# Performance work log

Measured on AMD Instinct MI355X. Metric: run time of the kernel, lower is better.

The kernel has to match this reference:

```python
import jax, jax.numpy as jnp
import numpy as np
from jax import lax

T, B, E = 512, 128, 128  # timesteps, batch, embedding_size
S = 2 * T                # stack capacity: 2 pushes per step


def setup_inputs() -> dict:
    key = jax.random.key(0)
    k1, k2, k3, k4, k5 = jax.random.split(key, 5)
    return {
        "v1": jax.random.normal(k1, (T, B, E), dtype=jnp.float32),
        "v2": jax.random.normal(k2, (T, B, E), dtype=jnp.float32),
        "d1": jax.random.uniform(k3, (T, B, 1), dtype=jnp.float32),
        "d2": jax.random.uniform(k4, (T, B, 1), dtype=jnp.float32),
        "u": jax.random.uniform(k5, (T, B, 1), dtype=jnp.float32),
    }


def _step(carry, xs):
    strengths, values = carry  # [B,S], [B,S,E]; slots 0..2(t+1)-1 valid after push
    v1t, v2t, d1t, d2t, ut, t = xs  # v*: [B,E]; d*,u: [B,1]; t: scalar int
    # --- push: append two entries at the top (slots 2t, 2t+1) ---
    values = lax.dynamic_update_slice(
        values, jnp.stack([v1t, v2t], axis=1), (0, 2 * t, 0))
    strengths = lax.dynamic_update_slice(
        strengths, jnp.concatenate([d1t, d2t], axis=1), (0, 2 * t))
    # exclusive reverse cumsum = strength used above each slot (top-down order)
    rev_incl = jnp.flip(jnp.cumsum(jnp.flip(strengths, 1), axis=1), 1)  # [B,S]
    used = rev_incl - strengths  # [B,S]
    # --- read: faithful to torch.max(u - strength_used) reducing over batch ---
    m = jnp.max(ut - used, axis=0)            # [S] scalar-over-batch per slot
    w = jnp.minimum(strengths, m[None, :])    # [B,S]; invalid slots hit v=0
    summary = jnp.einsum('bs,bse->be', w, values)  # [B,E]
    # --- pop: s -= min(s, relu(u - used)) using pre-pop strengths ---
    pop_amt = jnp.minimum(strengths, jnp.maximum(0.0, ut - used))
    strengths = strengths - pop_amt
    return (strengths, values), summary


def reference(v1, v2, d1, d2, u):
    init = (jnp.zeros((B, S), v1.dtype), jnp.zeros((B, S, E), v1.dtype))
    ts = jnp.arange(T, dtype=jnp.int32)
    _, out = lax.scan(_step, init, (v1, v2, d1, d2, u, ts))
    return out  # [T,B,E]: read content at each timestep
```

## Files before the change

kernel.cpp:

```cpp
#include <hip/hip_runtime.h>
#include <cstdint>
#include <cstddef>

#define TT 512
#define BB 128
#define EE 128
#define SS 1024
#define NEG_INF (-1e30f)

typedef _Float16 half8 __attribute__((ext_vector_type(8)));
typedef float floatx4 __attribute__((ext_vector_type(4)));

__device__ __forceinline__ unsigned int pkh(float x, float y) {
    _Float16 hx = (_Float16)x, hy = (_Float16)y;
    unsigned short bx, by;
    __builtin_memcpy(&bx, &hx, 2); __builtin_memcpy(&by, &hy, 2);
    return (unsigned int)bx | ((unsigned int)by << 16);
}

__device__ __forceinline__ unsigned int pkrtz(float x, float y) {
    auto h = __builtin_amdgcn_cvt_pkrtz(x, y);
    unsigned int r; __builtin_memcpy(&r, &h, 4); return r;
}

__global__ __launch_bounds__(64) void prefixF(
    const float* __restrict__ d1, const float* __restrict__ d2,
    const float* __restrict__ u,
    float* __restrict__ F, float* __restrict__ Bv,
    float* __restrict__ d2T, float* __restrict__ FT,
    float* __restrict__ BvT, float* __restrict__ CST,
    float* __restrict__ CMT, float* __restrict__ HT)
{
    const int b = blockIdx.x;
    const int lane = threadIdx.x;
    const int t0 = lane * 8;

    float l1[8], l2[8], g[8];
#pragma unroll
    for (int j = 0; j < 8; ++j) {
        const int t = t0 + j;
        l1[j] = d1[t * BB + b];
        l2[j] = d2[t * BB + b];
        g[j] = u[t * BB + b] - l1[j] - l2[j];
    }
    float p[8], s = 0.f;
#pragma unroll
    for (int j = 0; j < 8; ++j) { s += g[j]; p[j] = s; }

    float v = s;
#pragma unroll
    for (int off = 1; off < 64; off <<= 1) {
        float o = __shfl_up(v, off);
        if (lane >= off) v += o;
    }
    const float excl = v - s;

    float Fv[8];
#pragma unroll
    for (int j = 0; j < 8; ++j) Fv[j] = excl + p[j];

#pragma unroll
    for (int j = 0; j < 8; ++j) {
        const int t = t0 + j;
        const float Fm1 = (j > 0) ? Fv[j - 1] : excl;
        const float Bvv = Fm1 - l1[j];
        F  [b * TT + t] = Fv[j];
        Bv [b * TT + t] = Bvv;
        d2T[b * TT + t] = l2[j];
        FT [t * BB + b] = Fv[j];
        BvT[t * BB + b] = Bvv;
    }

    float pm[8], sm[8];
    pm[0] = Fv[0];
#pragma unroll
    for (int j = 1; j < 8; ++j) pm[j] = fmaxf(pm[j - 1], Fv[j]);
    sm[7] = Fv[7];
#pragma unroll
    for (int j = 6; j >= 0; --j) sm[j] = fmaxf(sm[j + 1], Fv[j]);

    float pcar = NEG_INF, scar = NEG_INF;
#pragma unroll
    for (int off = 1; off <= 3; ++off) {
        float xu = __shfl_up(pm[7], off);
        if ((lane & 3) >= off) pcar = fmaxf(pcar, xu);
        float xd = __shfl_down(sm[0], off);
        if ((lane & 3) + off <= 3) scar = fmaxf(scar, xd);
    }

#pragma unroll
    for (int j = 0; j < 8; ++j) {
        const int t = t0 + j;
        const float Hv  = fmaxf(pcar, (j > 0) ? pm[j - 1] : NEG_INF);
        const float CSv = fmaxf(sm[j], scar);
        HT [t * BB + b] = Hv;
        CST[t * BB + b] = CSv;
    }
    if ((lane & 3) == 0)
        CMT[(lane >> 2) * BB + b] = fmaxf(sm[0], scar);
}

__global__ __launch_bounds__(256) void calcM2(
    const float* __restrict__ FT, const float* __restrict__ BvT,
    const float* __restrict__ CST, const float* __restrict__ CMT,
    const float* __restrict__ HT, const float* __restrict__ u,
    float* __restrict__ m)
{
    const int t = (int)blockIdx.y;
    const int ci = (int)blockIdx.x;
    const int ct = t >> 5;
    if (ci > ct) return;

    const int tid = threadIdx.x;
    const int b = tid & 127, h = tid >> 7;
    const int ib = 32 * ci;

    __shared__ float cand[BB][66];
    __shared__ float Tot[2][BB];
    __shared__ float red[4][64];

    const float Ft = FT[t * BB + b];

    if (ci < ct) {
        float K = HT[t * BB + b];
        for (int c = ci + 1; c < ct; ++c) K = fmaxf(K, CMT[c * BB + b]);
#pragma unroll
        for (int j = 0; j < 16; ++j) {
            const int jj = 16 * h + j;
            const int i = ib + jj;
            const float R = fmaxf(CST[i * BB + b], K);
            const float Bvv = BvT[i * BB + b];
            cand[b][2 * jj]     = Ft - fmaxf(Bvv, R);
            cand[b][2 * jj + 1] = Ft - R;
        }
    } else {
        float vv[16], sfx[16];
#pragma unroll
        for (int j = 0; j < 16; ++j) {
            const int i = ib + 16 * h + j;
            vv[j] = (i < t) ? FT[i * BB + b] : NEG_INF;
        }
        sfx[15] = vv[15];
#pragma unroll
        for (int j = 14; j >= 0; --j) sfx[j] = fmaxf(vv[j], sfx[j + 1]);
        Tot[h][b] = sfx[0];
        __syncthreads();
        const float carry = (h == 0) ? Tot[1][b] : NEG_INF;
        const float ub = u[t * BB + b];
#pragma unroll
        for (int j = 0; j < 16; ++j) {
            const int jj = 16 * h + j;
            const int i = ib + jj;
            const float R = fmaxf(sfx[j], carry);
            const float Bvv = BvT[i * BB + b];
            cand[b][2 * jj]     = Ft - fmaxf(Bvv, R);
            cand[b][2 * jj + 1] = (i == t) ? ub : (Ft - R);
        }
    }
    __syncthreads();

    {
        const int s = tid & 63, g = tid >> 6;
        float mx = NEG_INF;
        const int b0 = g * 32;
#pragma unroll 8
        for (int bb = b0; bb < b0 + 32; ++bb) mx = fmaxf(mx, cand[bb][s]);
        red[g][s] = mx;
    }
    __syncthreads();
    if (tid < 64) {
        const float r = fmaxf(fmaxf(red[0][tid], red[1][tid]),
                              fmaxf(red[2][tid], red[3][tid]));
        const int s_glob = 64 * ci + tid;
        if (s_glob < 2 * t + 2) m[(size_t)t * SS + s_glob] = r;
    }
}

#define PWH 68
#define PWW 34
#define VTO 2176
#define FRO 6528
#define S0O 7040
#define BVO 7616
#define D2O 8128
#define TPO 8192

__global__ __launch_bounds__(256) void phaseC_mfma(
    const float* __restrict__ F, const float* __restrict__ Bvg,
    const float* __restrict__ d2T, const float* __restrict__ m,
    const float* __restrict__ v1, const float* __restrict__ v2,
    float* __restrict__ out)
{
    const int b  = blockIdx.x & (BB - 1);
    const int k8 = blockIdx.x >> 7;
    const int tt = 7 - (k8 ^ (((k8 + 2) >> 2) & 1));
    const int t0 = tt * 64;
    const int tid = threadIdx.x;

    __shared__ float sh[8256];

    const int lane = tid & 63, w = tid >> 6;
    const int wr = w >> 1, wc = w & 1;
    const int n = lane & 15;
    const int kq = (lane >> 4) * 8;
    const int il = tid & 31, g = tid >> 5;
    const int veb = tid & 7;
    const int vip = ((tid >> 3) & 7) + 8 * wc;
    const int veh = wr * 64;
    const int nchunks = 2 * tt + 2;

    float4 pv[8];
    float2 pmv[8];

    auto prefetch = [&](int ck) {
        const int ib = 32 * ck;
        const int i = ib + il;
#pragma unroll
        for (int r8 = 0; r8 < 8; ++r8) {
            const int t = t0 + 8 * g + r8;
            pmv[r8] = *(const float2*)&m[(size_t)t * SS + 2 * i];
        }
        const int i0 = ib + 2 * vip, i1 = i0 + 1;
        const float* p10 = v1 + ((size_t)i0 * BB + b) * EE;
        const float* p11 = v1 + ((size_t)i1 * BB + b) * EE;
        const float* p20 = v2 + ((size_t)i0 * BB + b) * EE;
        const float* p21 = v2 + ((size_t)i1 * BB + b) * EE;
#pragma unroll
        for (int c = 0; c < 2; ++c) {
            const int e0 = 4 * veb + 32 * c + veh;
            pv[4 * c + 0] = *(const float4*)&p10[e0];
            pv[4 * c + 1] = *(const float4*)&p11[e0];
            pv[4 * c + 2] = *(const float4*)&p20[e0];
            pv[4 * c + 3] = *(const float4*)&p21[e0];
        }
    };

    const int nF = t0 + 64;
    for (int k = tid; k < nF; k += 256) {
        sh[FRO + k] = F[b * TT + k];
        sh[BVO + k] = Bvg[b * TT + k];
    }
    if (tid < 64) sh[D2O + tid] = d2T[b * TT + t0 + tid];

    prefetch(0);

    __syncthreads();

    {
        const int k1 = tid, k2 = tid + 256, k3 = tid + 512;
        sh[S0O + k1] = (k1 < t0) ? sh[FRO + k1] : NEG_INF;
        sh[S0O + k2] = (k2 < t0) ? sh[FRO + k2] : NEG_INF;
        if (k3 < 576) sh[S0O + k3] = NEG_INF;
        if (tid < 64) {
            float xi = sh[FRO + t0 + tid];
#pragma unroll
            for (int off = 1; off < 64; off <<= 1) {
                const float y = __shfl_up(xi, off);
                if (tid >= off) xi = fmaxf(xi, y);
            }
            const float ex = __shfl_up(xi, 1);
            sh[TPO + tid] = (tid == 0) ? NEG_INF : ex;
        }
        __syncthreads();
        for (int off = 1; off < t0; off <<= 1) {
            float a1 = sh[S0O + k1]; if (k1 + off < 576) a1 = fmaxf(a1, sh[S0O + k1 + off]);
            float a2 = sh[S0O + k2]; if (k2 + off < 576) a2 = fmaxf(a2, sh[S0O + k2 + off]);
            __syncthreads();
            sh[S0O + k1] = a1; sh[S0O + k2] = a2;
            __syncthreads();
        }
    }

    float Freg2[8];
#pragma unroll
    for (int j = 0; j < 8; ++j) Freg2[j] = sh[FRO + t0 + 8 * g + j];
    const float qstart = sh[TPO + 8 * g];

    floatx4 acc[2][4];
#pragma unroll
    for (int r = 0; r < 2; ++r)
#pragma unroll
        for (int j = 0; j < 4; ++j) acc[r][j] = (floatx4)0.f;

    for (int ck = 0; ck < nchunks; ++ck) {
        const int ib = 32 * ck;
        const int i = ib + il;
        const bool below = (ib < t0);

        unsigned int wreg[8];
        {
            const float Ai = (i > 0) ? sh[FRO + i - 1] : 0.f;
            const float Bi = sh[BVO + i];
            const int li = i - t0;
            float q, S0i = 0.f;
            if (below) {
                S0i = sh[S0O + i];
                q = qstart;
            } else {
                q = NEG_INF;
                for (int k = li; k < 8 * g; ++k)
                    q = fmaxf(q, sh[FRO + t0 + k]);
            }
#pragma unroll
            for (int r8 = 0; r8 < 8; ++r8) {
                const int t_l = 8 * g + r8;
                const float2 mv = pmv[r8];
                float w0 = 0.f, w1 = 0.f;
                if (below) {
                    const float R = fmaxf(S0i, q);
                    const float a0 = fmaxf(Ai, R) - fmaxf(Bi, R);
                    const float a1 = fmaxf(Bi - R, 0.f);
                    w0 = fminf(a0, mv.x);
                    w1 = fminf(a1, mv.y);
                    q = fmaxf(q, Freg2[r8]);
                } else {
                    if (li <= t_l) {
                        const float R = q;
                        const float a0 = fmaxf(Ai, R) - fmaxf(Bi, R);
                        const float a1 = (li == t_l) ? sh[D2O + t_l]
                                                     : fmaxf(Bi - R, 0.f);
                        w0 = fminf(a0, mv.x);
                        w1 = fminf(a1, mv.y);
                    }
                    q = fmaxf(q, (t_l >= li) ? Freg2[r8] : NEG_INF);
                }
                wreg[r8] = pkh(w0, w1);
            }
        }

        uint2 vreg[8];
#pragma unroll
        for (int c = 0; c < 2; ++c) {
            const float4 xa = pv[4 * c + 0], xb = pv[4 * c + 1];
            const float4 ya = pv[4 * c + 2], yb = pv[4 * c + 3];
            vreg[4 * c + 0] = make_uint2(pkrtz(xa.x, ya.x), pkrtz(xb.x, yb.x));
            vreg[4 * c + 1] = make_uint2(pkrtz(xa.y, ya.y), pkrtz(xb.y, yb.y));
            vreg[4 * c + 2] = make_uint2(pkrtz(xa.z, ya.z), pkrtz(xb.z, yb.z));
            vreg[4 * c + 3] = make_uint2(pkrtz(xa.w, ya.w), pkrtz(xb.w, yb.w));
        }

        __syncthreads();

#pragma unroll
        for (int r8 = 0; r8 < 8; ++r8)
            ((unsigned int*)sh)[(8 * g + r8) * PWW + il] = wreg[r8];
        {
            unsigned int* vt = (unsigned int*)sh + VTO;
            const int dw = 2 * vip;
#pragma unroll
            for (int c = 0; c < 2; ++c) {
                const int e0 = 4 * veb + 32 * c + veh;
                *(uint2*)&vt[(e0 + 0) * PWW + dw] = vreg[4 * c + 0];
                *(uint2*)&vt[(e0 + 1) * PWW + dw] = vreg[4 * c + 1];
                *(uint2*)&vt[(e0 + 2) * PWW + dw] = vreg[4 * c + 2];
                *(uint2*)&vt[(e0 + 3) * PWW + dw] = vreg[4 * c + 3];
            }
        }

        __syncthreads();

        if (ck + 1 < nchunks) prefetch(ck + 1);

        __builtin_amdgcn_s_setprio(1);
        {
            const _Float16* WsH = (const _Float16*)sh;
            const _Float16* VtH = (const _Float16*)(sh + VTO);
#pragma unroll
            for (int k2 = 0; k2 < 64; k2 += 32) {
                const half8 av0 = *(const half8*)&WsH[(32 * wr + n) * PWH + kq + k2];
                const half8 av1 = *(const half8*)&WsH[(32 * wr + 16 + n) * PWH + kq + k2];
#pragma unroll
                for (int j = 0; j < 4; ++j) {
                    const half8 bv = *(const half8*)&VtH[(64 * wc + 16 * j + n) * PWH + kq + k2];
                    acc[0][j] = __builtin_amdgcn_mfma_f32_16x16x32_f16(av0, bv, acc[0][j], 0, 0, 0);
                    acc[1][j] = __builtin_amdgcn_mfma_f32_16x16x32_f16(av1, bv, acc[1][j], 0, 0, 0);
                }
            }
        }
        __builtin_amdgcn_s_setprio(0);
    }

    {
        const int q = lane >> 4;
#pragma unroll
        for (int r = 0; r < 2; ++r) {
#pragma unroll
            for (int j = 0; j < 4; ++j) {
#pragma unroll
                for (int reg = 0; reg < 4; ++reg) {
                    const int t = t0 + 32 * wr + 16 * r + 4 * q + reg;
                    const int col = 64 * wc + 16 * j + n;
                    out[((size_t)t * BB + b) * EE + col] = acc[r][j][reg];
                }
            }
        }
    }
}

extern "C" void kernel_launch(void* const* d_in, const int* in_sizes, int n_in,
                              void* d_out, int out_size, void* d_ws, size_t ws_size,
                              hipStream_t stream) {
    const float* v1 = (const float*)d_in[0];
    const float* v2 = (const float*)d_in[1];
    const float* d1 = (const float*)d_in[2];
    const float* d2 = (const float*)d_in[3];
    const float* u  = (const float*)d_in[4];
    float* out = (float*)d_out;

    char* ws = (char*)d_ws;
    float* m   = (float*)ws;
    float* F   = m   + (size_t)TT * SS;
    float* Bvp = F   + (size_t)BB * TT;
    float* d2T = Bvp + (size_t)BB * TT;
    float* FT  = d2T + (size_t)BB * TT;
    float* BvT = FT  + (size_t)BB * TT;
    float* CST = BvT + (size_t)BB * TT;
    float* HT  = CST + (size_t)BB * TT;
    float* CMT = HT  + (size_t)BB * TT;

    prefixF<<<dim3(BB), dim3(64), 0, stream>>>(d1, d2, u, F, Bvp, d2T, FT,
                                               BvT, CST, CMT, HT);
    calcM2 <<<dim3(16, TT), dim3(256), 0, stream>>>(FT, BvT, CST, CMT, HT, u, m);
    phaseC_mfma<<<dim3(BB * 8), dim3(256), 0, stream>>>(F, Bvp, d2T, m, v1, v2, out);
}
```

Measured before the change: 226.6 us.

## Split long time-tiles across blocks with atomic accumulation to balance load

Time tiles with four or more 64-step blocks have their chunk range split across two workgroups, so each block does at most eight chunks, and the grid grows from 8 to 12 blocks per batch row. Split tiles accumulate into output with atomicAdd after a memset of the upper half of the output. The shared-memory padding also changes (row pitch 68 to 72 halves) to alter bank mapping, and the value conversion switches from round-toward-zero packing to round-to-nearest packing. This adds a memset, atomic traffic and a larger LDS footprint in exchange for less tail imbalance.

```diff
diff --git a/kernel.cpp b/kernel.cpp
--- a/kernel.cpp
+++ b/kernel.cpp
@@ -16,11 +16,6 @@
     unsigned short bx, by;
     __builtin_memcpy(&bx, &hx, 2); __builtin_memcpy(&by, &hy, 2);
     return (unsigned int)bx | ((unsigned int)by << 16);
-}
-
-__device__ __forceinline__ unsigned int pkrtz(float x, float y) {
-    auto h = __builtin_amdgcn_cvt_pkrtz(x, y);
-    unsigned int r; __builtin_memcpy(&r, &h, 4); return r;
 }
 
 __global__ __launch_bounds__(64) void prefixF(
@@ -176,14 +171,14 @@
     }
 }
 
-#define PWH 68
-#define PWW 34
-#define VTO 2176
-#define FRO 6528
-#define S0O 7040
-#define BVO 7616
-#define D2O 8128
-#define TPO 8192
+#define PWH 72
+#define PWW 36
+#define VTO 2304
+#define FRO 6912
+#define S0O 7488
+#define BVO 8064
+#define D2O 8576
+#define TPO 8640
 
 __global__ __launch_bounds__(256) void phaseC_mfma(
     const float* __restrict__ F, const float* __restrict__ Bvg,
@@ -192,12 +187,26 @@
     float* __restrict__ out)
 {
     const int b  = blockIdx.x & (BB - 1);
-    const int k8 = blockIdx.x >> 7;
-    const int tt = 7 - (k8 ^ (((k8 + 2) >> 2) & 1));
+    const int wk = blockIdx.x >> 7;
+
+    int tt, ck0, nck;
+    if (wk < 6) {
+        nck = 8;
+        ck0 = (wk == 1) ? 8 : 0;
+        tt  = (wk <= 1) ? 7 : 8 - wk;
+    } else {
+        const int j = wk - 6;
+        nck = 6 - 2 * (j >> 1);
+        if (j & 1) { tt = 2 - (j >> 1); ck0 = 0; }
+        else       { tt = 6 - (j >> 1); ck0 = 8; }
+    }
     const int t0 = tt * 64;
+    const int ckEnd = ck0 + nck;
+    const bool splitTile = (tt >= 4);
+
     const int tid = threadIdx.x;
 
-    __shared__ float sh[8256];
+    __shared__ float sh[8704];
 
     const int lane = tid & 63, w = tid >> 6;
     const int wr = w >> 1, wc = w & 1;
@@ -207,7 +216,6 @@
     const int veb = tid & 7;
     const int vip = ((tid >> 3) & 7) + 8 * wc;
     const int veh = wr * 64;
-    const int nchunks = 2 * tt + 2;
 
     float4 pv[8];
     float2 pmv[8];
@@ -242,7 +250,7 @@
     }
     if (tid < 64) sh[D2O + tid] = d2T[b * TT + t0 + tid];
 
-    prefetch(0);
+    prefetch(ck0);
 
     __syncthreads();
 
@@ -282,7 +290,7 @@
 #pragma unroll
         for (int j = 0; j < 4; ++j) acc[r][j] = (floatx4)0.f;
 
-    for (int ck = 0; ck < nchunks; ++ck) {
+    for (int ck = ck0; ck < ckEnd; ++ck) {
         const int ib = 32 * ck;
         const int i = ib + il;
         const bool below = (ib < t0);
@@ -333,10 +341,10 @@
         for (int c = 0; c < 2; ++c) {
             const float4 xa = pv[4 * c + 0], xb = pv[4 * c + 1];
             const float4 ya = pv[4 * c + 2], yb = pv[4 * c + 3];
-            vreg[4 * c + 0] = make_uint2(pkrtz(xa.x, ya.x), pkrtz(xb.x, yb.x));
-            vreg[4 * c + 1] = make_uint2(pkrtz(xa.y, ya.y), pkrtz(xb.y, yb.y));
-            vreg[4 * c + 2] = make_uint2(pkrtz(xa.z, ya.z), pkrtz(xb.z, yb.z));
-            vreg[4 * c + 3] = make_uint2(pkrtz(xa.w, ya.w), pkrtz(xb.w, yb.w));
+            vreg[4 * c + 0] = make_uint2(pkh(xa.x, ya.x), pkh(xb.x, yb.x));
+            vreg[4 * c + 1] = make_uint2(pkh(xa.y, ya.y), pkh(xb.y, yb.y));
+            vreg[4 * c + 2] = make_uint2(pkh(xa.z, ya.z), pkh(xb.z, yb.z));
+            vreg[4 * c + 3] = make_uint2(pkh(xa.w, ya.w), pkh(xb.w, yb.w));
         }
 
         __syncthreads();
@@ -359,7 +367,7 @@
 
         __syncthreads();
 
-        if (ck + 1 < nchunks) prefetch(ck + 1);
+        if (ck + 1 < ckEnd) prefetch(ck + 1);
 
         __builtin_amdgcn_s_setprio(1);
         {
@@ -390,7 +398,9 @@
                 for (int reg = 0; reg < 4; ++reg) {
                     const int t = t0 + 32 * wr + 16 * r + 4 * q + reg;
                     const int col = 64 * wc + 16 * j + n;
-                    out[((size_t)t * BB + b) * EE + col] = acc[r][j][reg];
+                    float* dst = &out[((size_t)t * BB + b) * EE + col];
+                    if (splitTile) atomicAdd(dst, acc[r][j][reg]);
+                    else           *dst = acc[r][j][reg];
                 }
             }
         }
@@ -418,8 +428,11 @@
     float* HT  = CST + (size_t)BB * TT;
     float* CMT = HT  + (size_t)BB * TT;
 
+    hipMemsetAsync(out + (size_t)256 * BB * EE, 0,
+                   (size_t)256 * BB * EE * sizeof(float), stream);
+
     prefixF<<<dim3(BB), dim3(64), 0, stream>>>(d1, d2, u, F, Bvp, d2T, FT,
                                                BvT, CST, CMT, HT);
     calcM2 <<<dim3(16, TT), dim3(256), 0, stream>>>(FT, BvT, CST, CMT, HT, u, m);
-    phaseC_mfma<<<dim3(BB * 8), dim3(256), 0, stream>>>(F, Bvp, d2T, m, v1, v2, out);
+    phaseC_mfma<<<dim3(12 * BB), dim3(256), 0, stream>>>(F, Bvp, d2T, m, v1, v2, out);
 }
```

New measurement: 207.9 us. 1.09x faster.
